# Performance work log

Measured on AMD Instinct MI355X. Metric: run time of the kernel, lower is better.

The kernel has to match this reference:

```python
import jax, jax.numpy as jnp
import numpy as np

EPSILON = 1e-7  # wl-coref utils.add_dummy epsilon
LEAKY_SLOPE = 0.01  # torch.nn.LeakyReLU default

N_MENTIONS = 10000
BATCH = 512
N_ANTS = 50
MENTION_EMB = 1024
PW_EMB = 64
IN_FEATURES = 3 * MENTION_EMB + PW_EMB  # 3136
HIDDEN = 128


def setup_inputs() -> dict:
    key = jax.random.key(0)
    ks = jax.random.split(key, 9)
    return {
        "all_mentions": jax.random.normal(ks[0], (N_MENTIONS, MENTION_EMB), jnp.float32),
        "mentions_batch": jax.random.normal(ks[1], (BATCH, MENTION_EMB), jnp.float32),
        "pw_batch": jax.random.normal(ks[2], (BATCH, N_ANTS, PW_EMB), jnp.float32),
        "top_indices_batch": jax.random.randint(ks[3], (BATCH, N_ANTS), 0, N_MENTIONS, jnp.int64 if jax.config.jax_enable_x64 else jnp.int32),
        "top_rough_scores_batch": jax.random.normal(ks[4], (BATCH, N_ANTS), jnp.float32),
        "W1": jax.random.normal(ks[5], (IN_FEATURES, HIDDEN), jnp.float32) * 0.02,
        "b1": jax.random.normal(ks[6], (HIDDEN,), jnp.float32) * 0.02,
        "W_out": jax.random.normal(ks[7], (HIDDEN, 1), jnp.float32) * 0.02,
        "b_out": jax.random.normal(ks[8], (1,), jnp.float32) * 0.02,
    }


def reference(all_mentions, mentions_batch, pw_batch, top_indices_batch,
              top_rough_scores_batch, W1, b1, W_out, b_out):
    batch, n_ants = top_indices_batch.shape
    emb = mentions_batch.shape[1]
    # pair matrix: [batch, n_ants, 3*emb + pw_emb]
    a_mentions = jnp.broadcast_to(mentions_batch[:, None, :], (batch, n_ants, emb))
    b_mentions = all_mentions[top_indices_batch]          # gather: [batch, n_ants, emb]
    similarity = a_mentions * b_mentions
    pair_matrix = jnp.concatenate((a_mentions, b_mentions, similarity, pw_batch), axis=2)
    # FFNN: Linear -> LeakyReLU -> (Dropout=identity in eval) -> Linear(out=1)
    h = jax.nn.leaky_relu(jnp.einsum('baf,fh->bah', pair_matrix, W1) + b1, LEAKY_SLOPE)
    ffnn = (jnp.einsum('bah,ho->bao', h, W_out) + b_out)[..., 0]  # [batch, n_ants]
    scores = top_rough_scores_batch + ffnn
    # add_dummy(eps=True): prepend a column of EPSILON
    dummy = jnp.full((batch, 1), EPSILON, dtype=scores.dtype)
    return jnp.concatenate((dummy, scores), axis=1)  # [batch, n_ants + 1]
```

## Files before the change

### kernel.cpp

```cpp
#include <hip/hip_runtime.h>

#define N_MENT   10000
#define BATCH    512
#define N_ANTS   50
#define EMB      1024
#define PW_EMB   64
#define IN_F     3136
#define HID      128
#define M_TOT    (BATCH * N_ANTS)
#define EPS_VAL  1e-7f
#define SLOPE    0.01f

#define NKT      98
#define CONV_BLK 196
#define MAIN_BLK BATCH

using f32x4 = __attribute__((ext_vector_type(4))) float;
using s16x8 = __attribute__((ext_vector_type(8))) short;
using u16x8 = __attribute__((ext_vector_type(8))) unsigned short;

__device__ __forceinline__ unsigned short f2bf(float f) {
  unsigned u = __builtin_bit_cast(unsigned, f);
  u += 0x7FFFu + ((u >> 16) & 1u);
  return (unsigned short)(u >> 16);
}

__device__ __forceinline__ u16x8 pack8(float4 lo, float4 hi) {
  union { u16x8 v; unsigned u[4]; } r;
  asm("v_cvt_pk_bf16_f32 %0, %1, %2" : "=v"(r.u[0]) : "v"(lo.x), "v"(lo.y));
  asm("v_cvt_pk_bf16_f32 %0, %1, %2" : "=v"(r.u[1]) : "v"(lo.z), "v"(lo.w));
  asm("v_cvt_pk_bf16_f32 %0, %1, %2" : "=v"(r.u[2]) : "v"(hi.x), "v"(hi.y));
  asm("v_cvt_pk_bf16_f32 %0, %1, %2" : "=v"(r.u[3]) : "v"(hi.z), "v"(hi.w));
  return r.v;
}

__device__ __forceinline__ float4 fmul4(float4 a, float4 b) {
  return make_float4(a.x * b.x, a.y * b.y, a.z * b.z, a.w * b.w);
}

__device__ __forceinline__ int tile_orig_k(int tk) {
  if (tk >= 96) return 3072 + (tk - 96) * 32;
  const int c = tk / 6, r = tk % 6;
  return (r >> 1) * 1024 + c * 64 + (r & 1) * 32;
}

__global__ __launch_bounds__(256) void k_convert(const float* __restrict__ w1,
                                                 unsigned short* __restrict__ w1f) {
  const int id   = blockIdx.x * 256 + threadIdx.x;
  const int lane = id & 63;
  const int tile = id >> 6;
  const int tk   = tile % NKT, tn = tile / NKT;
  const int n    = tn * 16 + (lane & 15);
  const int k    = tile_orig_k(tk) + (lane >> 4) * 8;
  u16x8 o;
  #pragma unroll
  for (int j = 0; j < 8; ++j) o[j] = f2bf(w1[(size_t)(k + j) * HID + n]);
  *(u16x8*)(w1f + (size_t)id * 8) = o;
}

__global__ __launch_bounds__(512) void k_main(
    const float* __restrict__ all_m, const float* __restrict__ men,
    const float* __restrict__ pw, const int* __restrict__ topi,
    const float* __restrict__ rough, const unsigned short* __restrict__ w1f,
    const float* __restrict__ b1, const float* __restrict__ wout,
    const float* __restrict__ bout, float* __restrict__ out) {
  __shared__ __align__(16) unsigned short Xs[2][3][64 * 64];
  __shared__ float red[8][64];

  const int t   = threadIdx.x;
  const int bid = blockIdx.x;
  const int mbase = bid * N_ANTS;

  const int sr = t >> 3, sq = t & 7;
  const int r  = sr < N_ANTS ? sr : N_ANTS - 1;
  const int m  = mbase + r;
  const int bidx = topi[m];
  const float* pA = men   + (size_t)bid  * EMB    + sq * 8;
  const float* pB = all_m + (size_t)bidx * EMB    + sq * 8;
  const float* pP = pw    + (size_t)m    * PW_EMB + sq * 8;
  const int widx = sr * 64 + (((sq * 16) ^ ((sr & 7) << 4)) >> 1);

  const int lane = t & 63, wid = t >> 6;
  const int ln = lane & 15, lg = lane >> 4;
  const unsigned short* wf = w1f + (size_t)wid * NKT * 512 + lane * 8;

  int ridx[2][4];
  #pragma unroll
  for (int ks = 0; ks < 2; ++ks)
    #pragma unroll
    for (int mt = 0; mt < 4; ++mt) {
      const int R = mt * 16 + ln;
      ridx[ks][mt] = R * 64 + (((ks * 64 + lg * 16) ^ ((R & 7) << 4)) >> 1);
    }

  f32x4 acc[4] = {};

  float4 av0 = ((const float4*)pA)[0], av1 = ((const float4*)pA)[1];
  float4 bv0 = ((const float4*)pB)[0], bv1 = ((const float4*)pB)[1];

  s16x8 wcur[6], wnext[6];
  #pragma unroll
  for (int j = 0; j < 6; ++j)
    wcur[j] = *(const s16x8*)(wf + (size_t)j * 512);

  int buf = 0;
  for (int c = 0; c < 16; ++c) {
    *(u16x8*)&Xs[buf][0][widx] = pack8(av0, av1);
    *(u16x8*)&Xs[buf][1][widx] = pack8(bv0, bv1);
    *(u16x8*)&Xs[buf][2][widx] = pack8(fmul4(av0, bv0), fmul4(av1, bv1));

    if (c < 15) {
      const float* qA = pA + (c + 1) * 64;
      const float* qB = pB + (c + 1) * 64;
      av0 = ((const float4*)qA)[0]; av1 = ((const float4*)qA)[1];
      bv0 = ((const float4*)qB)[0]; bv1 = ((const float4*)qB)[1];
    } else {
      av0 = ((const float4*)pP)[0]; av1 = ((const float4*)pP)[1];
    }

    #pragma unroll
    for (int j = 0; j < 6; ++j) {
      const int tkn = (c < 15) ? (c + 1) * 6 + j : (j < 2 ? 96 + j : 97);
      wnext[j] = *(const s16x8*)(wf + (size_t)tkn * 512);
    }

    __syncthreads();
    #pragma unroll
    for (int j = 0; j < 6; ++j) {
      const int reg = j >> 1, ks = j & 1;
      #pragma unroll
      for (int mt = 0; mt < 4; ++mt) {
        s16x8 x = *(const s16x8*)&Xs[buf][reg][ridx[ks][mt]];
        acc[mt] = __builtin_amdgcn_mfma_f32_16x16x32_bf16(x, wcur[j], acc[mt], 0, 0, 0);
      }
    }
    #pragma unroll
    for (int j = 0; j < 6; ++j) wcur[j] = wnext[j];
    buf ^= 1;
  }

  {
    *(u16x8*)&Xs[buf][0][widx] = pack8(av0, av1);
    __syncthreads();
    #pragma unroll
    for (int ks = 0; ks < 2; ++ks)
      #pragma unroll
      for (int mt = 0; mt < 4; ++mt) {
        s16x8 x = *(const s16x8*)&Xs[buf][0][ridx[ks][mt]];
        acc[mt] = __builtin_amdgcn_mfma_f32_16x16x32_bf16(x, wcur[ks], acc[mt], 0, 0, 0);
      }
  }

  const int n0 = wid * 16 + ln;
  const float bias = b1[n0], w_o = wout[n0];
  #pragma unroll
  for (int mt = 0; mt < 4; ++mt)
    #pragma unroll
    for (int e = 0; e < 4; ++e) {
      float h = acc[mt][e] + bias;
      h = h > 0.f ? h : SLOPE * h;
      float ss = h * w_o;
      ss += __shfl_xor(ss, 1);
      ss += __shfl_xor(ss, 2);
      ss += __shfl_xor(ss, 4);
      ss += __shfl_xor(ss, 8);
      if (ln == 0) red[wid][mt * 16 + lg * 4 + e] = ss;
    }
  __syncthreads();
  if (t < N_ANTS) {
    const int gm = mbase + t;
    float v = red[0][t];
    #pragma unroll
    for (int w = 1; w < 8; ++w) v += red[w][t];
    out[(size_t)bid * (N_ANTS + 1) + 1 + t] = rough[gm] + v + bout[0];
  }
  if (t == 0) out[(size_t)bid * (N_ANTS + 1)] = EPS_VAL;
}

__global__ void k_eps(float* __restrict__ out) {
  out[(size_t)threadIdx.x * (N_ANTS + 1)] = EPS_VAL;
}

__global__ __launch_bounds__(128) void k_fb(const float* __restrict__ all_m,
                                            const float* __restrict__ men,
                                            const float* __restrict__ pw,
                                            const int*   __restrict__ topi,
                                            const float* __restrict__ rough,
                                            const float* __restrict__ w1,
                                            const float* __restrict__ b1,
                                            const float* __restrict__ wout,
                                            const float* __restrict__ bout,
                                            float* __restrict__ out) {
  __shared__ float xs[IN_F];
  __shared__ float hred[HID];
  const int pair = blockIdx.x;
  const int t = threadIdx.x;
  const int bb = pair / N_ANTS;
  const int idx = topi[pair];
  const float* pA = men + (size_t)bb * EMB;
  const float* pB = all_m + (size_t)idx * EMB;
  for (int k = t; k < EMB; k += 128) {
    float a = pA[k], b = pB[k];
    xs[k] = a; xs[EMB + k] = b; xs[2 * EMB + k] = a * b;
  }
  if (t < PW_EMB) xs[3 * EMB + t] = pw[(size_t)pair * PW_EMB + t];
  __syncthreads();
  float acc = 0.f;
  for (int k = 0; k < IN_F; ++k) acc = fmaf(xs[k], w1[(size_t)k * HID + t], acc);
  acc += b1[t];
  acc = acc > 0.f ? acc : SLOPE * acc;
  hred[t] = acc * wout[t];
  __syncthreads();
  for (int off = 64; off > 0; off >>= 1) {
    if (t < off) hred[t] += hred[t + off];
    __syncthreads();
  }
  if (t == 0)
    out[(size_t)bb * (N_ANTS + 1) + 1 + (pair - bb * N_ANTS)] = rough[pair] + hred[0] + bout[0];
}

extern "C" void kernel_launch(void* const* d_in, const int* in_sizes, int n_in,
                              void* d_out, int out_size, void* d_ws, size_t ws_size,
                              hipStream_t stream) {
  const float* all_m = (const float*)d_in[0];
  const float* men   = (const float*)d_in[1];
  const float* pw    = (const float*)d_in[2];
  const int*   topi  = (const int*)  d_in[3];
  const float* rough = (const float*)d_in[4];
  const float* w1    = (const float*)d_in[5];
  const float* b1    = (const float*)d_in[6];
  const float* wout  = (const float*)d_in[7];
  const float* bout  = (const float*)d_in[8];
  float* out = (float*)d_out;

  const size_t W1F_BYTES = (size_t)HID * IN_F * sizeof(unsigned short);

  if (ws_size >= W1F_BYTES) {
    unsigned short* w1f = (unsigned short*)d_ws;
    k_convert<<<CONV_BLK, 256, 0, stream>>>(w1, w1f);
    k_main<<<MAIN_BLK, 512, 0, stream>>>(all_m, men, pw, topi, rough, w1f,
                                         b1, wout, bout, out);
  } else {
    k_eps<<<1, BATCH, 0, stream>>>(out);
    k_fb<<<M_TOT, 128, 0, stream>>>(all_m, men, pw, topi, rough, w1, b1, wout, bout, out);
  }
}
```

Before: 44.56 us.

## Hoist broadcast mention term out of per-pair GEMM as per-row bias

The mention embedding is identical for all 50 antecedents of a batch row, so its contribution to W1 is computed once per block as a 128-wide fp32 vector (scalar FMAs over W1 from global memory) and folded into the bias. The MFMA loop then only processes the b and a*b slices plus pw, cutting about a third of the matrix work and LDS staging. Warps are also remapped to a 2x2 tile layout (two N-tiles by two M halves) to reuse A fragments across two weight columns. The per-block fp32 dot over 1024x128 weights adds global traffic and serial FMA latency.

New measurement: 53.18 us. 1.19x slower.

```diff
diff --git a/kernel.cpp b/kernel.cpp
--- a/kernel.cpp
+++ b/kernel.cpp
@@ -62,14 +62,20 @@
     const float* __restrict__ all_m, const float* __restrict__ men,
     const float* __restrict__ pw, const int* __restrict__ topi,
     const float* __restrict__ rough, const unsigned short* __restrict__ w1f,
-    const float* __restrict__ b1, const float* __restrict__ wout,
-    const float* __restrict__ bout, float* __restrict__ out) {
-  __shared__ __align__(16) unsigned short Xs[2][3][64 * 64];
-  __shared__ float red[8][64];
+    const float* __restrict__ w1, const float* __restrict__ b1,
+    const float* __restrict__ wout, const float* __restrict__ bout,
+    float* __restrict__ out) {
+  __shared__ __align__(16) unsigned short Xs[2][2][64 * 64];
+  __shared__ float aLDS[EMB];
+  __shared__ float yred[4][HID];
+  __shared__ float red[4][64];
 
   const int t   = threadIdx.x;
   const int bid = blockIdx.x;
   const int mbase = bid * N_ANTS;
+
+  aLDS[t]       = men[(size_t)bid * EMB + t];
+  aLDS[t + 512] = men[(size_t)bid * EMB + t + 512];
 
   const int sr = t >> 3, sq = t & 7;
   const int r  = sr < N_ANTS ? sr : N_ANTS - 1;
@@ -82,32 +88,35 @@
 
   const int lane = t & 63, wid = t >> 6;
   const int ln = lane & 15, lg = lane >> 4;
-  const unsigned short* wf = w1f + (size_t)wid * NKT * 512 + lane * 8;
-
-  int ridx[2][4];
+  const int np = wid & 3, mh = wid >> 2;
+  const unsigned short* wf0 = w1f + (size_t)(2 * np)     * NKT * 512 + lane * 8;
+  const unsigned short* wf1 = w1f + (size_t)(2 * np + 1) * NKT * 512 + lane * 8;
+
+  int ridx[2][2];
   #pragma unroll
   for (int ks = 0; ks < 2; ++ks)
     #pragma unroll
-    for (int mt = 0; mt < 4; ++mt) {
-      const int R = mt * 16 + ln;
+    for (int mt = 0; mt < 2; ++mt) {
+      const int R = mh * 32 + mt * 16 + ln;
       ridx[ks][mt] = R * 64 + (((ks * 64 + lg * 16) ^ ((R & 7) << 4)) >> 1);
     }
 
-  f32x4 acc[4] = {};
+  f32x4 acc[2][2] = {};
 
   float4 av0 = ((const float4*)pA)[0], av1 = ((const float4*)pA)[1];
   float4 bv0 = ((const float4*)pB)[0], bv1 = ((const float4*)pB)[1];
 
-  s16x8 wcur[6], wnext[6];
-  #pragma unroll
-  for (int j = 0; j < 6; ++j)
-    wcur[j] = *(const s16x8*)(wf + (size_t)j * 512);
+  s16x8 wcur[2][4], wnext[2][4];
+  #pragma unroll
+  for (int j = 0; j < 4; ++j) {
+    wcur[0][j] = *(const s16x8*)(wf0 + (size_t)(2 + j) * 512);
+    wcur[1][j] = *(const s16x8*)(wf1 + (size_t)(2 + j) * 512);
+  }
 
   int buf = 0;
   for (int c = 0; c < 16; ++c) {
-    *(u16x8*)&Xs[buf][0][widx] = pack8(av0, av1);
-    *(u16x8*)&Xs[buf][1][widx] = pack8(bv0, bv1);
-    *(u16x8*)&Xs[buf][2][widx] = pack8(fmul4(av0, bv0), fmul4(av1, bv1));
+    *(u16x8*)&Xs[buf][0][widx] = pack8(bv0, bv1);
+    *(u16x8*)&Xs[buf][1][widx] = pack8(fmul4(av0, bv0), fmul4(av1, bv1));
 
     if (c < 15) {
       const float* qA = pA + (c + 1) * 64;
@@ -119,23 +128,25 @@
     }
 
     #pragma unroll
-    for (int j = 0; j < 6; ++j) {
-      const int tkn = (c < 15) ? (c + 1) * 6 + j : (j < 2 ? 96 + j : 97);
-      wnext[j] = *(const s16x8*)(wf + (size_t)tkn * 512);
+    for (int j = 0; j < 4; ++j) {
+      const int tkn = (c < 15) ? (c + 1) * 6 + 2 + j : 96 + (j & 1);
+      wnext[0][j] = *(const s16x8*)(wf0 + (size_t)tkn * 512);
+      wnext[1][j] = *(const s16x8*)(wf1 + (size_t)tkn * 512);
     }
 
     __syncthreads();
     #pragma unroll
-    for (int j = 0; j < 6; ++j) {
+    for (int j = 0; j < 4; ++j) {
       const int reg = j >> 1, ks = j & 1;
-      #pragma unroll
-      for (int mt = 0; mt < 4; ++mt) {
-        s16x8 x = *(const s16x8*)&Xs[buf][reg][ridx[ks][mt]];
-        acc[mt] = __builtin_amdgcn_mfma_f32_16x16x32_bf16(x, wcur[j], acc[mt], 0, 0, 0);
-      }
-    }
-    #pragma unroll
-    for (int j = 0; j < 6; ++j) wcur[j] = wnext[j];
+      s16x8 x0 = *(const s16x8*)&Xs[buf][reg][ridx[ks][0]];
+      s16x8 x1 = *(const s16x8*)&Xs[buf][reg][ridx[ks][1]];
+      acc[0][0] = __builtin_amdgcn_mfma_f32_16x16x32_bf16(x0, wcur[0][j], acc[0][0], 0, 0, 0);
+      acc[0][1] = __builtin_amdgcn_mfma_f32_16x16x32_bf16(x0, wcur[1][j], acc[0][1], 0, 0, 0);
+      acc[1][0] = __builtin_amdgcn_mfma_f32_16x16x32_bf16(x1, wcur[0][j], acc[1][0], 0, 0, 0);
+      acc[1][1] = __builtin_amdgcn_mfma_f32_16x16x32_bf16(x1, wcur[1][j], acc[1][1], 0, 0, 0);
+    }
+    #pragma unroll
+    for (int j = 0; j < 4; ++j) { wcur[0][j] = wnext[0][j]; wcur[1][j] = wnext[1][j]; }
     buf ^= 1;
   }
 
@@ -143,35 +154,52 @@
     *(u16x8*)&Xs[buf][0][widx] = pack8(av0, av1);
     __syncthreads();
     #pragma unroll
-    for (int ks = 0; ks < 2; ++ks)
-      #pragma unroll
-      for (int mt = 0; mt < 4; ++mt) {
-        s16x8 x = *(const s16x8*)&Xs[buf][0][ridx[ks][mt]];
-        acc[mt] = __builtin_amdgcn_mfma_f32_16x16x32_bf16(x, wcur[ks], acc[mt], 0, 0, 0);
-      }
-  }
-
-  const int n0 = wid * 16 + ln;
-  const float bias = b1[n0], w_o = wout[n0];
-  #pragma unroll
-  for (int mt = 0; mt < 4; ++mt)
+    for (int ks = 0; ks < 2; ++ks) {
+      s16x8 x0 = *(const s16x8*)&Xs[buf][0][ridx[ks][0]];
+      s16x8 x1 = *(const s16x8*)&Xs[buf][0][ridx[ks][1]];
+      acc[0][0] = __builtin_amdgcn_mfma_f32_16x16x32_bf16(x0, wcur[0][ks], acc[0][0], 0, 0, 0);
+      acc[0][1] = __builtin_amdgcn_mfma_f32_16x16x32_bf16(x0, wcur[1][ks], acc[0][1], 0, 0, 0);
+      acc[1][0] = __builtin_amdgcn_mfma_f32_16x16x32_bf16(x1, wcur[0][ks], acc[1][0], 0, 0, 0);
+      acc[1][1] = __builtin_amdgcn_mfma_f32_16x16x32_bf16(x1, wcur[1][ks], acc[1][1], 0, 0, 0);
+    }
+  }
+
+  {
+    const int gn = t & 127, kq = t >> 7;
+    const float* wcol = w1 + gn;
+    const float* ap = aLDS + kq * 256;
+    float part = 0.f;
+    #pragma unroll 8
+    for (int k = 0; k < 256; ++k)
+      part = fmaf(ap[k], wcol[(size_t)(kq * 256 + k) * HID], part);
+    yred[kq][gn] = part;
+  }
+  __syncthreads();
+
+  const int n0 = np * 32 + ln, n1 = np * 32 + 16 + ln;
+  const float ya0 = yred[0][n0] + yred[1][n0] + yred[2][n0] + yred[3][n0];
+  const float ya1 = yred[0][n1] + yred[1][n1] + yred[2][n1] + yred[3][n1];
+  const float bias0 = b1[n0] + ya0, bias1 = b1[n1] + ya1;
+  const float w_0 = wout[n0], w_1 = wout[n1];
+  #pragma unroll
+  for (int mt = 0; mt < 2; ++mt)
     #pragma unroll
     for (int e = 0; e < 4; ++e) {
-      float h = acc[mt][e] + bias;
-      h = h > 0.f ? h : SLOPE * h;
-      float ss = h * w_o;
+      float h0 = acc[mt][0][e] + bias0;
+      float h1 = acc[mt][1][e] + bias1;
+      h0 = h0 > 0.f ? h0 : SLOPE * h0;
+      h1 = h1 > 0.f ? h1 : SLOPE * h1;
+      float ss = h0 * w_0 + h1 * w_1;
       ss += __shfl_xor(ss, 1);
       ss += __shfl_xor(ss, 2);
       ss += __shfl_xor(ss, 4);
       ss += __shfl_xor(ss, 8);
-      if (ln == 0) red[wid][mt * 16 + lg * 4 + e] = ss;
+      if (ln == 0) red[np][mh * 32 + mt * 16 + lg * 4 + e] = ss;
     }
   __syncthreads();
   if (t < N_ANTS) {
     const int gm = mbase + t;
-    float v = red[0][t];
-    #pragma unroll
-    for (int w = 1; w < 8; ++w) v += red[w][t];
+    const float v = red[0][t] + red[1][t] + red[2][t] + red[3][t];
     out[(size_t)bid * (N_ANTS + 1) + 1 + t] = rough[gm] + v + bout[0];
   }
   if (t == 0) out[(size_t)bid * (N_ANTS + 1)] = EPS_VAL;
@@ -238,7 +266,7 @@
   if (ws_size >= W1F_BYTES) {
     unsigned short* w1f = (unsigned short*)d_ws;
     k_convert<<<CONV_BLK, 256, 0, stream>>>(w1, w1f);
-    k_main<<<MAIN_BLK, 512, 0, stream>>>(all_m, men, pw, topi, rough, w1f,
+    k_main<<<MAIN_BLK, 512, 0, stream>>>(all_m, men, pw, topi, rough, w1f, w1,
                                          b1, wout, bout, out);
   } else {
     k_eps<<<1, BATCH, 0, stream>>>(out);
```

## Hoist broadcast mention term out of per-pair GEMM into per-block bias

Applied to the files above, without the earlier changes.

The mentions_batch row is identical for all 50 antecedents in a block, so its W1 contribution is computed once per block as a matrix-vector product and folded into the bias. The MFMA loop now covers only the b and a*b segments, cutting its MFMA work and LDS staging by a third and shrinking shared memory. The trade is a serial scalar dot-product tail per wave that reloads weight fragments from global memory.

Result: slower. 46.46 us (+4.3%).

```diff
diff --git a/kernel.cpp b/kernel.cpp
--- a/kernel.cpp
+++ b/kernel.cpp
@@ -64,7 +64,7 @@
     const float* __restrict__ rough, const unsigned short* __restrict__ w1f,
     const float* __restrict__ b1, const float* __restrict__ wout,
     const float* __restrict__ bout, float* __restrict__ out) {
-  __shared__ __align__(16) unsigned short Xs[2][3][64 * 64];
+  __shared__ __align__(16) unsigned short Xs[2][2][64 * 64];
   __shared__ float red[8][64];
 
   const int t   = threadIdx.x;
@@ -98,16 +98,15 @@
   float4 av0 = ((const float4*)pA)[0], av1 = ((const float4*)pA)[1];
   float4 bv0 = ((const float4*)pB)[0], bv1 = ((const float4*)pB)[1];
 
-  s16x8 wcur[6], wnext[6];
-  #pragma unroll
-  for (int j = 0; j < 6; ++j)
-    wcur[j] = *(const s16x8*)(wf + (size_t)j * 512);
+  s16x8 wcur[4], wnext[4];
+  #pragma unroll
+  for (int j = 0; j < 4; ++j)
+    wcur[j] = *(const s16x8*)(wf + (size_t)(2 + j) * 512);
 
   int buf = 0;
   for (int c = 0; c < 16; ++c) {
-    *(u16x8*)&Xs[buf][0][widx] = pack8(av0, av1);
-    *(u16x8*)&Xs[buf][1][widx] = pack8(bv0, bv1);
-    *(u16x8*)&Xs[buf][2][widx] = pack8(fmul4(av0, bv0), fmul4(av1, bv1));
+    *(u16x8*)&Xs[buf][0][widx] = pack8(bv0, bv1);
+    *(u16x8*)&Xs[buf][1][widx] = pack8(fmul4(av0, bv0), fmul4(av1, bv1));
 
     if (c < 15) {
       const float* qA = pA + (c + 1) * 64;
@@ -119,14 +118,14 @@
     }
 
     #pragma unroll
-    for (int j = 0; j < 6; ++j) {
-      const int tkn = (c < 15) ? (c + 1) * 6 + j : (j < 2 ? 96 + j : 97);
+    for (int j = 0; j < 4; ++j) {
+      const int tkn = (c < 15) ? (c + 1) * 6 + 2 + j : 96 + (j & 1);
       wnext[j] = *(const s16x8*)(wf + (size_t)tkn * 512);
     }
 
     __syncthreads();
     #pragma unroll
-    for (int j = 0; j < 6; ++j) {
+    for (int j = 0; j < 4; ++j) {
       const int reg = j >> 1, ks = j & 1;
       #pragma unroll
       for (int mt = 0; mt < 4; ++mt) {
@@ -135,7 +134,7 @@
       }
     }
     #pragma unroll
-    for (int j = 0; j < 6; ++j) wcur[j] = wnext[j];
+    for (int j = 0; j < 4; ++j) wcur[j] = wnext[j];
     buf ^= 1;
   }
 
@@ -151,8 +150,35 @@
       }
   }
 
+  float ya = 0.f;
+  {
+    const float* aU = men + (size_t)bid * EMB + lg * 8;
+    #pragma unroll 4
+    for (int c2 = 0; c2 < 32; ++c2) {
+      const int cc = c2 >> 1, ks = c2 & 1;
+      u16x8 fr = *(const u16x8*)(wf + (size_t)(cc * 6 + ks) * 512);
+      const float* ap = aU + cc * 64 + ks * 32;
+      float4 a0 = *(const float4*)ap;
+      float4 a1 = *(const float4*)(ap + 4);
+      float w0 = __builtin_bit_cast(float, (unsigned)fr[0] << 16);
+      float w1v = __builtin_bit_cast(float, (unsigned)fr[1] << 16);
+      float w2 = __builtin_bit_cast(float, (unsigned)fr[2] << 16);
+      float w3 = __builtin_bit_cast(float, (unsigned)fr[3] << 16);
+      float w4 = __builtin_bit_cast(float, (unsigned)fr[4] << 16);
+      float w5 = __builtin_bit_cast(float, (unsigned)fr[5] << 16);
+      float w6 = __builtin_bit_cast(float, (unsigned)fr[6] << 16);
+      float w7 = __builtin_bit_cast(float, (unsigned)fr[7] << 16);
+      ya = fmaf(w0, a0.x, ya); ya = fmaf(w1v, a0.y, ya);
+      ya = fmaf(w2, a0.z, ya); ya = fmaf(w3, a0.w, ya);
+      ya = fmaf(w4, a1.x, ya); ya = fmaf(w5, a1.y, ya);
+      ya = fmaf(w6, a1.z, ya); ya = fmaf(w7, a1.w, ya);
+    }
+    ya += __shfl_xor(ya, 16);
+    ya += __shfl_xor(ya, 32);
+  }
+
   const int n0 = wid * 16 + ln;
-  const float bias = b1[n0], w_o = wout[n0];
+  const float bias = b1[n0] + ya, w_o = wout[n0];
   #pragma unroll
   for (int mt = 0; mt < 4; ++mt)
     #pragma unroll
```
